# Performance work log

Measured on AMD Instinct MI355X. Metric: run time of the kernel, lower is better.

The kernel has to match this reference:

```python
import jax, jax.numpy as jnp
import numpy as np

D_TXT, D_IMG, D_C, K, N = 768, 1024, 256, 10, 200000
H, HD = 4, 64  # num_heads, head_dim (D_C = H*HD)


def _ln(x, g, b):
    m = x.mean(-1, keepdims=True)
    v = ((x - m) ** 2).mean(-1, keepdims=True)
    return (x - m) / jnp.sqrt(v + 1e-5) * g + b


def _proj(x, W, b, g, be):
    # Linear -> LayerNorm -> ReLU (the *_proj_completion blocks)
    return jax.nn.relu(_ln(x @ W.T + b, g, be))


def setup_inputs() -> dict:
    key = jax.random.key(0)
    ks = jax.random.split(key, 16)
    s = 0.02
    p = lambda i, shape: jax.random.normal(ks[i], shape, jnp.float32) * s
    z = lambda: jnp.zeros((D_C,), jnp.float32)
    o = lambda: jnp.ones((D_C,), jnp.float32)
    return {
        "query": jax.random.normal(ks[0], (D_TXT,), jnp.float32),
        "cand_text": jax.random.normal(ks[1], (N, D_TXT), jnp.float32),
        "cand_img": jax.random.normal(ks[2], (N, D_IMG), jnp.float32),
        "proto_feat": jax.random.normal(ks[3], (D_C,), jnp.float32),
        "W_txt": p(4, (D_C, D_TXT)), "b_txt": z(), "g_txt": o(), "be_txt": z(),
        "W_img": p(5, (D_C, D_IMG)), "b_img": z(), "g_img": o(), "be_img": z(),
        "Wq": p(6, (D_C, D_C)), "bq": z(),
        "Wk": p(7, (D_C, D_C)), "bk": z(),
        "Wv": p(8, (D_C, D_C)), "bv": z(),
        "Wo": p(9, (D_C, D_C)), "bo": z(),
        "g1": o(), "be1": z(),
        "W1": p(10, (4 * D_C, D_C)), "b1": jnp.zeros((4 * D_C,), jnp.float32),
        "W2": p(11, (D_C, 4 * D_C)), "b2": z(),
        "g2": o(), "be2": z(),
        "k": K,
    }


def reference(query, cand_text, cand_img, proto_feat,
              W_txt, b_txt, g_txt, be_txt,
              W_img, b_img, g_img, be_img,
              Wq, bq, Wk, bk, Wv, bv, Wo, bo,
              g1, be1, W1, b1, W2, b2, g2, be2, k):
    # ---- search_neighbors: cosine sim + topk over the available (text) DB ----
    qn = query / jnp.maximum(jnp.linalg.norm(query), 1e-12)
    cn = cand_text / jnp.maximum(
        jnp.linalg.norm(cand_text, axis=1, keepdims=True), 1e-12)
    sims = cn @ qn                                  # [N]
    _, idx = jax.lax.top_k(sims, k)                 # [k]
    neigh_txt = cand_text[idx]                      # [k, D_TXT]
    neigh_img = cand_img[idx]                       # [k, D_IMG]

    # ---- complete_feature ----
    avail_feat = _proj(query, W_txt, b_txt, g_txt, be_txt)        # [D_C]
    avail_nb = _proj(neigh_txt, W_txt, b_txt, g_txt, be_txt)      # [k, D_C]
    miss_nb = _proj(neigh_img, W_img, b_img, g_img, be_img)       # [k, D_C]

    Kmat = jnp.concatenate([proto_feat[None], avail_nb], axis=0)  # [k+1, D_C]
    Vmat = jnp.concatenate([proto_feat[None], miss_nb], axis=0)   # [k+1, D_C]

    qp = (avail_feat @ Wq.T + bq).reshape(H, HD)                  # [H, HD]
    kp = (Kmat @ Wk.T + bk).reshape(-1, H, HD)                    # [k+1, H, HD]
    vp = (Vmat @ Wv.T + bv).reshape(-1, H, HD)                    # [k+1, H, HD]
    scores = jnp.einsum('hd,nhd->hn', qp, kp) / jnp.sqrt(
        jnp.asarray(HD, jnp.float32))                             # [H, k+1]
    attn = jax.nn.softmax(scores, axis=-1)
    ctx = jnp.einsum('hn,nhd->hd', attn, vp).reshape(D_C)
    attn_out = ctx @ Wo.T + bo                                    # [D_C]

    out = _ln(attn_out + proto_feat, g1, be1)
    ffn = jax.nn.relu(out @ W1.T + b1) @ W2.T + b2
    out = _ln(ffn + out, g2, be2) + proto_feat
    return out
```

## Files before the change

kernel.cpp:

```cpp
#include <hip/hip_runtime.h>
#include <cfloat>
#include <climits>
#include <math.h>

#define N_CAND 200000
#define DTXT 768
#define DIMG 1024
#define DC 256
#define KTOP 10
#define NKV 11
#define CHUNK 2000
#define NBLK_TOPK 100

__device__ __forceinline__ float wave_sum(float v) {
#pragma unroll
  for (int off = 32; off; off >>= 1) v += __shfl_xor(v, off, 64);
  return v;
}

__global__ void k_sims(const float* __restrict__ q, const float* __restrict__ ct,
                       float* __restrict__ sims) {
  const int lane = threadIdx.x & 63;
  const int wave = threadIdx.x >> 6;
  const int row = blockIdx.x * 4 + wave;
  if (row >= N_CAND) return;
  const float4* r4 = (const float4*)(ct + (size_t)row * DTXT);
  const float4* q4 = (const float4*)q;
  float dot = 0.f, nrm = 0.f;
#pragma unroll
  for (int i = 0; i < 3; ++i) {
    float4 a = r4[lane + i * 64];
    float4 b = q4[lane + i * 64];
    dot += a.x * b.x + a.y * b.y + a.z * b.z + a.w * b.w;
    nrm += a.x * a.x + a.y * a.y + a.z * a.z + a.w * a.w;
  }
  dot = wave_sum(dot);
  nrm = wave_sum(nrm);
  if (lane == 0) sims[row] = dot / fmaxf(sqrtf(nrm), 1e-12f);
}

__device__ int block_argmax_pos(float* sv, const int* si, int M) {
  const int t = threadIdx.x;
  __shared__ float wv[4];
  __shared__ int wp[4];
  float bv = -FLT_MAX;
  int bp = -1;
  for (int j = t; j < M; j += 256) {
    float v = sv[j];
    if (bp < 0 || v > bv || (v == bv && si[j] < si[bp])) { bv = v; bp = j; }
  }
#pragma unroll
  for (int off = 32; off; off >>= 1) {
    float ov = __shfl_xor(bv, off, 64);
    int op = __shfl_xor(bp, off, 64);
    if (op >= 0 && (bp < 0 || ov > bv || (ov == bv && si[op] < si[bp]))) {
      bv = ov; bp = op;
    }
  }
  if ((t & 63) == 0) { wv[t >> 6] = bv; wp[t >> 6] = bp; }
  __syncthreads();
  if (t == 0) {
#pragma unroll
    for (int w = 1; w < 4; ++w) {
      if (wp[w] >= 0 && (wp[0] < 0 || wv[w] > wv[0] ||
                         (wv[w] == wv[0] && si[wp[w]] < si[wp[0]]))) {
        wv[0] = wv[w]; wp[0] = wp[w];
      }
    }
  }
  __syncthreads();
  int res = wp[0];
  __syncthreads();
  return res;
}

__global__ void k_topk_part(const float* __restrict__ sims,
                            float* __restrict__ cvals, int* __restrict__ cidx) {
  __shared__ float sv[CHUNK];
  __shared__ int si[CHUNK];
  const int t = threadIdx.x;
  const int lo = blockIdx.x * CHUNK;
  for (int j = t; j < CHUNK; j += 256) { sv[j] = sims[lo + j]; si[j] = lo + j; }
  __syncthreads();
  for (int r = 0; r < KTOP; ++r) {
    int p = block_argmax_pos(sv, si, CHUNK);
    if (t == 0) {
      cvals[blockIdx.x * KTOP + r] = sv[p];
      cidx[blockIdx.x * KTOP + r] = si[p];
      sv[p] = -INFINITY;
    }
    __syncthreads();
  }
}

__global__ void k_topk_final(const float* __restrict__ cvals,
                             const int* __restrict__ cidx,
                             int* __restrict__ fidx) {
  __shared__ float sv[NBLK_TOPK * KTOP];
  __shared__ int si[NBLK_TOPK * KTOP];
  const int t = threadIdx.x;
  for (int j = t; j < NBLK_TOPK * KTOP; j += 256) { sv[j] = cvals[j]; si[j] = cidx[j]; }
  __syncthreads();
  for (int r = 0; r < KTOP; ++r) {
    int p = block_argmax_pos(sv, si, NBLK_TOPK * KTOP);
    if (t == 0) { fidx[r] = si[p]; sv[p] = -INFINITY; }
    __syncthreads();
  }
}

__global__ void k_proj(const float* __restrict__ q, const float* __restrict__ ct,
                       const float* __restrict__ ci,
                       const float* __restrict__ Wt, const float* __restrict__ bt,
                       const float* __restrict__ gt, const float* __restrict__ bet,
                       const float* __restrict__ Wi, const float* __restrict__ bi,
                       const float* __restrict__ gi, const float* __restrict__ bei,
                       const int* __restrict__ fidx,
                       float* __restrict__ af, float* __restrict__ anb,
                       float* __restrict__ mnb) {
  __shared__ float x[DIMG];
  __shared__ float tmp[DC];
  __shared__ float redm, redr;
  const int t = threadIdx.x;
  const int j = blockIdx.x;
  const float *W, *b, *g, *be, *src;
  float* dst;
  int D;
  if (j == 0) {
    src = q; D = DTXT; W = Wt; b = bt; g = gt; be = bet; dst = af;
  } else if (j < 11) {
    src = ct + (size_t)fidx[j - 1] * DTXT;
    D = DTXT; W = Wt; b = bt; g = gt; be = bet; dst = anb + (j - 1) * DC;
  } else {
    src = ci + (size_t)fidx[j - 11] * DIMG;
    D = DIMG; W = Wi; b = bi; g = gi; be = bei; dst = mnb + (j - 11) * DC;
  }
  for (int d = t; d < D; d += 256) x[d] = src[d];
  __syncthreads();
  const float4* w4 = (const float4*)(W + (size_t)t * D);
  float acc = 0.f;
  for (int d4 = 0; d4 < (D >> 2); ++d4) {
    float4 w = w4[d4];
    acc += w.x * x[4 * d4] + w.y * x[4 * d4 + 1] + w.z * x[4 * d4 + 2] +
           w.w * x[4 * d4 + 3];
  }
  acc += b[t];
  tmp[t] = acc;
  __syncthreads();
  if (t < 64) {
    float s = tmp[t] + tmp[t + 64] + tmp[t + 128] + tmp[t + 192];
    s = wave_sum(s);
    if (t == 0) redm = s * (1.f / 256.f);
  }
  __syncthreads();
  if (t < 64) {
    float s = 0.f;
#pragma unroll
    for (int kk = 0; kk < 4; ++kk) {
      float d0 = tmp[t + 64 * kk] - redm;
      s += d0 * d0;
    }
    s = wave_sum(s);
    if (t == 0) redr = rsqrtf(s * (1.f / 256.f) + 1e-5f);
  }
  __syncthreads();
  float y = (acc - redm) * redr * g[t] + be[t];
  dst[t] = fmaxf(y, 0.f);
}

__global__ void __launch_bounds__(1024) k_attn_ffn(
    const float* __restrict__ proto, const float* __restrict__ Wq,
    const float* __restrict__ bq, const float* __restrict__ Wk,
    const float* __restrict__ bk, const float* __restrict__ Wv,
    const float* __restrict__ bv, const float* __restrict__ Wo,
    const float* __restrict__ bo, const float* __restrict__ g1,
    const float* __restrict__ be1, const float* __restrict__ W1,
    const float* __restrict__ b1, const float* __restrict__ W2,
    const float* __restrict__ b2, const float* __restrict__ g2,
    const float* __restrict__ be2, const float* __restrict__ af,
    const float* __restrict__ anb, const float* __restrict__ mnb,
    float* __restrict__ out) {
  __shared__ float s_af[DC];
  __shared__ float s_K[NKV * DC];
  __shared__ float s_V[NKV * DC];
  __shared__ float s_qp[DC];
  __shared__ float s_kp[NKV * DC];
  __shared__ float s_vp[NKV * DC];
  __shared__ float s_sc[4][NKV];
  __shared__ float s_at[4][NKV];
  __shared__ float s_ctx[DC];
  __shared__ float s_t[DC];
  __shared__ float s_o1[DC];
  __shared__ float s_h[4 * DC];
  __shared__ float redm, redr;
  const int t = threadIdx.x;

  if (t < DC) {
    s_af[t] = af[t];
    s_K[t] = proto[t];
    s_V[t] = proto[t];
  }
  for (int i = t; i < KTOP * DC; i += 1024) {
    s_K[DC + i] = anb[i];
    s_V[DC + i] = mnb[i];
  }
  __syncthreads();

  if (t < DC) {
    const float4* w4 = (const float4*)(Wq + (size_t)t * DC);
    float a = 0.f;
    for (int d4 = 0; d4 < DC / 4; ++d4) {
      float4 w = w4[d4];
      a += w.x * s_af[4 * d4] + w.y * s_af[4 * d4 + 1] +
           w.z * s_af[4 * d4 + 2] + w.w * s_af[4 * d4 + 3];
    }
    s_qp[t] = a + bq[t];
  }
  for (int o = t; o < NKV * DC; o += 1024) {
    int n = o >> 8, c = o & 255;
    const float4* wk4 = (const float4*)(Wk + (size_t)c * DC);
    const float4* wv4 = (const float4*)(Wv + (size_t)c * DC);
    const float* Kn = s_K + n * DC;
    const float* Vn = s_V + n * DC;
    float ak = 0.f, av = 0.f;
    for (int d4 = 0; d4 < DC / 4; ++d4) {
      float4 wk_ = wk4[d4], wv_ = wv4[d4];
      ak += wk_.x * Kn[4 * d4] + wk_.y * Kn[4 * d4 + 1] +
            wk_.z * Kn[4 * d4 + 2] + wk_.w * Kn[4 * d4 + 3];
      av += wv_.x * Vn[4 * d4] + wv_.y * Vn[4 * d4 + 1] +
            wv_.z * Vn[4 * d4 + 2] + wv_.w * Vn[4 * d4 + 3];
    }
    s_kp[o] = ak + bk[c];
    s_vp[o] = av + bv[c];
  }
  __syncthreads();

  if (t < 4 * NKV) {
    int h = t / NKV, n = t % NKV;
    const float* qh = s_qp + h * 64;
    const float* kh = s_kp + n * DC + h * 64;
    float a = 0.f;
#pragma unroll
    for (int d = 0; d < 64; ++d) a += qh[d] * kh[d];
    s_sc[h][n] = a * 0.125f;
  }
  __syncthreads();
  if (t < 4) {
    float m = -INFINITY;
    for (int n = 0; n < NKV; ++n) m = fmaxf(m, s_sc[t][n]);
    float s = 0.f;
    for (int n = 0; n < NKV; ++n) {
      float e = expf(s_sc[t][n] - m);
      s_at[t][n] = e;
      s += e;
    }
    float inv = 1.f / s;
    for (int n = 0; n < NKV; ++n) s_at[t][n] *= inv;
  }
  __syncthreads();
  if (t < DC) {
    int h = t >> 6;
    float a = 0.f;
#pragma unroll
    for (int n = 0; n < NKV; ++n) a += s_at[h][n] * s_vp[n * DC + t];
    s_ctx[t] = a;
  }
  __syncthreads();
  float myv = 0.f;
  if (t < DC) {
    const float4* w4 = (const float4*)(Wo + (size_t)t * DC);
    float a = 0.f;
    for (int d4 = 0; d4 < DC / 4; ++d4) {
      float4 w = w4[d4];
      a += w.x * s_ctx[4 * d4] + w.y * s_ctx[4 * d4 + 1] +
           w.z * s_ctx[4 * d4 + 2] + w.w * s_ctx[4 * d4 + 3];
    }
    myv = a + bo[t] + proto[t];
    s_t[t] = myv;
  }
  __syncthreads();
  if (t < 64) {
    float s = s_t[t] + s_t[t + 64] + s_t[t + 128] + s_t[t + 192];
    s = wave_sum(s);
    if (t == 0) redm = s * (1.f / 256.f);
  }
  __syncthreads();
  if (t < 64) {
    float s = 0.f;
#pragma unroll
    for (int kk = 0; kk < 4; ++kk) {
      float d0 = s_t[t + 64 * kk] - redm;
      s += d0 * d0;
    }
    s = wave_sum(s);
    if (t == 0) redr = rsqrtf(s * (1.f / 256.f) + 1e-5f);
  }
  __syncthreads();
  if (t < DC) s_o1[t] = (myv - redm) * redr * g1[t] + be1[t];
  __syncthreads();
  {
    const float4* w4 = (const float4*)(W1 + (size_t)t * DC);
    float a = 0.f;
    for (int d4 = 0; d4 < DC / 4; ++d4) {
      float4 w = w4[d4];
      a += w.x * s_o1[4 * d4] + w.y * s_o1[4 * d4 + 1] +
           w.z * s_o1[4 * d4 + 2] + w.w * s_o1[4 * d4 + 3];
    }
    s_h[t] = fmaxf(a + b1[t], 0.f);
  }
  __syncthreads();
  float myy = 0.f;
  if (t < DC) {
    const float4* w4 = (const float4*)(W2 + (size_t)t * 4 * DC);
    float a = 0.f;
    for (int d4 = 0; d4 < DC; ++d4) {
      float4 w = w4[d4];
      a += w.x * s_h[4 * d4] + w.y * s_h[4 * d4 + 1] +
           w.z * s_h[4 * d4 + 2] + w.w * s_h[4 * d4 + 3];
    }
    myy = a + b2[t] + s_o1[t];
    s_t[t] = myy;
  }
  __syncthreads();
  if (t < 64) {
    float s = s_t[t] + s_t[t + 64] + s_t[t + 128] + s_t[t + 192];
    s = wave_sum(s);
    if (t == 0) redm = s * (1.f / 256.f);
  }
  __syncthreads();
  if (t < 64) {
    float s = 0.f;
#pragma unroll
    for (int kk = 0; kk < 4; ++kk) {
      float d0 = s_t[t + 64 * kk] - redm;
      s += d0 * d0;
    }
    s = wave_sum(s);
    if (t == 0) redr = rsqrtf(s * (1.f / 256.f) + 1e-5f);
  }
  __syncthreads();
  if (t < DC) out[t] = (myy - redm) * redr * g2[t] + be2[t] + proto[t];
}

extern "C" void kernel_launch(void* const* d_in, const int* in_sizes, int n_in,
                              void* d_out, int out_size, void* d_ws,
                              size_t ws_size, hipStream_t stream) {
  (void)in_sizes; (void)n_in; (void)out_size; (void)ws_size;
  const float* query = (const float*)d_in[0];
  const float* ct    = (const float*)d_in[1];
  const float* ci    = (const float*)d_in[2];
  const float* proto = (const float*)d_in[3];
  const float* Wt    = (const float*)d_in[4];
  const float* bt    = (const float*)d_in[5];
  const float* gt    = (const float*)d_in[6];
  const float* bet   = (const float*)d_in[7];
  const float* Wi    = (const float*)d_in[8];
  const float* bi    = (const float*)d_in[9];
  const float* gi    = (const float*)d_in[10];
  const float* bei   = (const float*)d_in[11];
  const float* Wq    = (const float*)d_in[12];
  const float* bq    = (const float*)d_in[13];
  const float* Wk    = (const float*)d_in[14];
  const float* bk    = (const float*)d_in[15];
  const float* Wv    = (const float*)d_in[16];
  const float* bv    = (const float*)d_in[17];
  const float* Wo    = (const float*)d_in[18];
  const float* bo    = (const float*)d_in[19];
  const float* g1    = (const float*)d_in[20];
  const float* be1   = (const float*)d_in[21];
  const float* W1    = (const float*)d_in[22];
  const float* b1    = (const float*)d_in[23];
  const float* W2    = (const float*)d_in[24];
  const float* b2    = (const float*)d_in[25];
  const float* g2    = (const float*)d_in[26];
  const float* be2   = (const float*)d_in[27];
  float* out = (float*)d_out;

  char* ws = (char*)d_ws;
  float* sims  = (float*)(ws);
  float* cvals = (float*)(ws + 800000);
  int*   cidx  = (int*)(ws + 804000);
  int*   fidx  = (int*)(ws + 808000);
  float* af    = (float*)(ws + 808064);
  float* anb   = (float*)(ws + 809088);
  float* mnb   = (float*)(ws + 819328);

  k_sims<<<dim3(N_CAND / 4), dim3(256), 0, stream>>>(query, ct, sims);
  k_topk_part<<<dim3(NBLK_TOPK), dim3(256), 0, stream>>>(sims, cvals, cidx);
  k_topk_final<<<dim3(1), dim3(256), 0, stream>>>(cvals, cidx, fidx);
  k_proj<<<dim3(21), dim3(256), 0, stream>>>(query, ct, ci, Wt, bt, gt, bet, Wi,
                                             bi, gi, bei, fidx, af, anb, mnb);
  k_attn_ffn<<<dim3(1), dim3(1024), 0, stream>>>(
      proto, Wq, bq, Wk, bk, Wv, bv, Wo, bo, g1, be1, W1, b1, W2, b2, g2, be2,
      af, anb, mnb, out);
}
```

Before: 1.586 ms.

## Split single-block attention/FFN kernel into multi-block stage kernels

Replaces the single 1024-thread block that did QKV projection, attention, output projection and FFN with six smaller kernels. QKV runs over 23 blocks, and Wo, W1 and W2 are split across several blocks, so the matrix-vector work is spread over more compute units. The cost is extra launches and intermediate results passing through global workspace memory. The single-block tail was likely latency-bound by serial weight reads.

```diff
diff --git a/kernel.cpp b/kernel.cpp
--- a/kernel.cpp
+++ b/kernel.cpp
@@ -167,73 +167,55 @@
   dst[t] = fmaxf(y, 0.f);
 }
 
-__global__ void __launch_bounds__(1024) k_attn_ffn(
-    const float* __restrict__ proto, const float* __restrict__ Wq,
-    const float* __restrict__ bq, const float* __restrict__ Wk,
-    const float* __restrict__ bk, const float* __restrict__ Wv,
-    const float* __restrict__ bv, const float* __restrict__ Wo,
-    const float* __restrict__ bo, const float* __restrict__ g1,
-    const float* __restrict__ be1, const float* __restrict__ W1,
-    const float* __restrict__ b1, const float* __restrict__ W2,
-    const float* __restrict__ b2, const float* __restrict__ g2,
-    const float* __restrict__ be2, const float* __restrict__ af,
-    const float* __restrict__ anb, const float* __restrict__ mnb,
-    float* __restrict__ out) {
-  __shared__ float s_af[DC];
-  __shared__ float s_K[NKV * DC];
-  __shared__ float s_V[NKV * DC];
+__global__ void k_qkv(const float* __restrict__ proto,
+                      const float* __restrict__ Wq, const float* __restrict__ bq,
+                      const float* __restrict__ Wk, const float* __restrict__ bk,
+                      const float* __restrict__ Wv, const float* __restrict__ bv,
+                      const float* __restrict__ af, const float* __restrict__ anb,
+                      const float* __restrict__ mnb,
+                      float* __restrict__ qp, float* __restrict__ kp,
+                      float* __restrict__ vp) {
+  __shared__ float x[DC];
+  const int t = threadIdx.x;
+  const int j = blockIdx.x;
+  const float *W, *b, *src;
+  float* dst;
+  if (j == 0) {
+    W = Wq; b = bq; src = af; dst = qp;
+  } else if (j < 12) {
+    const int n = j - 1;
+    W = Wk; b = bk; src = (n == 0) ? proto : anb + (n - 1) * DC;
+    dst = kp + n * DC;
+  } else {
+    const int n = j - 12;
+    W = Wv; b = bv; src = (n == 0) ? proto : mnb + (n - 1) * DC;
+    dst = vp + n * DC;
+  }
+  x[t] = src[t];
+  __syncthreads();
+  const float4* w4 = (const float4*)(W + (size_t)t * DC);
+  float a = 0.f;
+  for (int d4 = 0; d4 < DC / 4; ++d4) {
+    float4 w = w4[d4];
+    a += w.x * x[4 * d4] + w.y * x[4 * d4 + 1] + w.z * x[4 * d4 + 2] +
+         w.w * x[4 * d4 + 3];
+  }
+  dst[t] = a + b[t];
+}
+
+__global__ void k_score_ctx(const float* __restrict__ qp,
+                            const float* __restrict__ kp,
+                            const float* __restrict__ vp,
+                            float* __restrict__ ctx) {
   __shared__ float s_qp[DC];
   __shared__ float s_kp[NKV * DC];
   __shared__ float s_vp[NKV * DC];
   __shared__ float s_sc[4][NKV];
   __shared__ float s_at[4][NKV];
-  __shared__ float s_ctx[DC];
-  __shared__ float s_t[DC];
-  __shared__ float s_o1[DC];
-  __shared__ float s_h[4 * DC];
-  __shared__ float redm, redr;
-  const int t = threadIdx.x;
-
-  if (t < DC) {
-    s_af[t] = af[t];
-    s_K[t] = proto[t];
-    s_V[t] = proto[t];
-  }
-  for (int i = t; i < KTOP * DC; i += 1024) {
-    s_K[DC + i] = anb[i];
-    s_V[DC + i] = mnb[i];
-  }
-  __syncthreads();
-
-  if (t < DC) {
-    const float4* w4 = (const float4*)(Wq + (size_t)t * DC);
-    float a = 0.f;
-    for (int d4 = 0; d4 < DC / 4; ++d4) {
-      float4 w = w4[d4];
-      a += w.x * s_af[4 * d4] + w.y * s_af[4 * d4 + 1] +
-           w.z * s_af[4 * d4 + 2] + w.w * s_af[4 * d4 + 3];
-    }
-    s_qp[t] = a + bq[t];
-  }
-  for (int o = t; o < NKV * DC; o += 1024) {
-    int n = o >> 8, c = o & 255;
-    const float4* wk4 = (const float4*)(Wk + (size_t)c * DC);
-    const float4* wv4 = (const float4*)(Wv + (size_t)c * DC);
-    const float* Kn = s_K + n * DC;
-    const float* Vn = s_V + n * DC;
-    float ak = 0.f, av = 0.f;
-    for (int d4 = 0; d4 < DC / 4; ++d4) {
-      float4 wk_ = wk4[d4], wv_ = wv4[d4];
-      ak += wk_.x * Kn[4 * d4] + wk_.y * Kn[4 * d4 + 1] +
-            wk_.z * Kn[4 * d4 + 2] + wk_.w * Kn[4 * d4 + 3];
-      av += wv_.x * Vn[4 * d4] + wv_.y * Vn[4 * d4 + 1] +
-            wv_.z * Vn[4 * d4 + 2] + wv_.w * Vn[4 * d4 + 3];
-    }
-    s_kp[o] = ak + bk[c];
-    s_vp[o] = av + bv[c];
-  }
-  __syncthreads();
-
+  const int t = threadIdx.x;
+  s_qp[t] = qp[t];
+  for (int i = t; i < NKV * DC; i += 256) { s_kp[i] = kp[i]; s_vp[i] = vp[i]; }
+  __syncthreads();
   if (t < 4 * NKV) {
     int h = t / NKV, n = t % NKV;
     const float* qh = s_qp + h * 64;
@@ -257,26 +239,42 @@
     for (int n = 0; n < NKV; ++n) s_at[t][n] *= inv;
   }
   __syncthreads();
-  if (t < DC) {
+  {
     int h = t >> 6;
     float a = 0.f;
 #pragma unroll
     for (int n = 0; n < NKV; ++n) a += s_at[h][n] * s_vp[n * DC + t];
-    s_ctx[t] = a;
-  }
-  __syncthreads();
-  float myv = 0.f;
-  if (t < DC) {
-    const float4* w4 = (const float4*)(Wo + (size_t)t * DC);
-    float a = 0.f;
-    for (int d4 = 0; d4 < DC / 4; ++d4) {
-      float4 w = w4[d4];
-      a += w.x * s_ctx[4 * d4] + w.y * s_ctx[4 * d4 + 1] +
-           w.z * s_ctx[4 * d4 + 2] + w.w * s_ctx[4 * d4 + 3];
-    }
-    myv = a + bo[t] + proto[t];
-    s_t[t] = myv;
-  }
+    ctx[t] = a;
+  }
+}
+
+__global__ void k_wo(const float* __restrict__ Wo, const float* __restrict__ bo,
+                     const float* __restrict__ proto,
+                     const float* __restrict__ ctx, float* __restrict__ t1) {
+  __shared__ float s_c[DC];
+  const int t = threadIdx.x;
+  ((float4*)s_c)[t] = ((const float4*)ctx)[t];
+  __syncthreads();
+  const int c = blockIdx.x * 64 + t;
+  const float4* w4 = (const float4*)(Wo + (size_t)c * DC);
+  float a = 0.f;
+  for (int d4 = 0; d4 < DC / 4; ++d4) {
+    float4 w = w4[d4];
+    a += w.x * s_c[4 * d4] + w.y * s_c[4 * d4 + 1] + w.z * s_c[4 * d4 + 2] +
+         w.w * s_c[4 * d4 + 3];
+  }
+  t1[c] = a + bo[c] + proto[c];
+}
+
+__global__ void k_ffn1(const float* __restrict__ g1, const float* __restrict__ be1,
+                       const float* __restrict__ W1, const float* __restrict__ b1,
+                       const float* __restrict__ t1, float* __restrict__ o1w,
+                       float* __restrict__ h) {
+  __shared__ float s_t[DC];
+  __shared__ float s_o1[DC];
+  __shared__ float redm, redr;
+  const int t = threadIdx.x;
+  s_t[t] = t1[t];
   __syncthreads();
   if (t < 64) {
     float s = s_t[t] + s_t[t + 64] + s_t[t + 128] + s_t[t + 192];
@@ -295,31 +293,49 @@
     if (t == 0) redr = rsqrtf(s * (1.f / 256.f) + 1e-5f);
   }
   __syncthreads();
-  if (t < DC) s_o1[t] = (myv - redm) * redr * g1[t] + be1[t];
-  __syncthreads();
-  {
-    const float4* w4 = (const float4*)(W1 + (size_t)t * DC);
+  s_o1[t] = (s_t[t] - redm) * redr * g1[t] + be1[t];
+  __syncthreads();
+  if (blockIdx.x == 0) o1w[t] = s_o1[t];
+  if (t < 128) {
+    const int o = blockIdx.x * 128 + t;
+    const float4* w4 = (const float4*)(W1 + (size_t)o * DC);
     float a = 0.f;
     for (int d4 = 0; d4 < DC / 4; ++d4) {
       float4 w = w4[d4];
       a += w.x * s_o1[4 * d4] + w.y * s_o1[4 * d4 + 1] +
            w.z * s_o1[4 * d4 + 2] + w.w * s_o1[4 * d4 + 3];
     }
-    s_h[t] = fmaxf(a + b1[t], 0.f);
-  }
-  __syncthreads();
-  float myy = 0.f;
-  if (t < DC) {
-    const float4* w4 = (const float4*)(W2 + (size_t)t * 4 * DC);
-    float a = 0.f;
-    for (int d4 = 0; d4 < DC; ++d4) {
-      float4 w = w4[d4];
-      a += w.x * s_h[4 * d4] + w.y * s_h[4 * d4 + 1] +
-           w.z * s_h[4 * d4 + 2] + w.w * s_h[4 * d4 + 3];
-    }
-    myy = a + b2[t] + s_o1[t];
-    s_t[t] = myy;
-  }
+    h[o] = fmaxf(a + b1[o], 0.f);
+  }
+}
+
+__global__ void k_ffn2(const float* __restrict__ W2, const float* __restrict__ b2,
+                       const float* __restrict__ o1w, const float* __restrict__ h,
+                       float* __restrict__ t2) {
+  __shared__ float s_h[4 * DC];
+  const int t = threadIdx.x;
+#pragma unroll
+  for (int i = 0; i < 4; ++i)
+    ((float4*)s_h)[t + 64 * i] = ((const float4*)h)[t + 64 * i];
+  __syncthreads();
+  const int c = blockIdx.x * 64 + t;
+  const float4* w4 = (const float4*)(W2 + (size_t)c * 4 * DC);
+  float a = 0.f;
+  for (int d4 = 0; d4 < DC; ++d4) {
+    float4 w = w4[d4];
+    a += w.x * s_h[4 * d4] + w.y * s_h[4 * d4 + 1] + w.z * s_h[4 * d4 + 2] +
+         w.w * s_h[4 * d4 + 3];
+  }
+  t2[c] = a + b2[c] + o1w[c];
+}
+
+__global__ void k_ln2(const float* __restrict__ g2, const float* __restrict__ be2,
+                      const float* __restrict__ proto,
+                      const float* __restrict__ t2, float* __restrict__ out) {
+  __shared__ float s_t[DC];
+  __shared__ float redm, redr;
+  const int t = threadIdx.x;
+  s_t[t] = t2[t];
   __syncthreads();
   if (t < 64) {
     float s = s_t[t] + s_t[t + 64] + s_t[t + 128] + s_t[t + 192];
@@ -338,7 +354,7 @@
     if (t == 0) redr = rsqrtf(s * (1.f / 256.f) + 1e-5f);
   }
   __syncthreads();
-  if (t < DC) out[t] = (myy - redm) * redr * g2[t] + be2[t] + proto[t];
+  out[t] = (s_t[t] - redm) * redr * g2[t] + be2[t] + proto[t];
 }
 
 extern "C" void kernel_launch(void* const* d_in, const int* in_sizes, int n_in,
@@ -383,13 +399,25 @@
   float* af    = (float*)(ws + 808064);
   float* anb   = (float*)(ws + 809088);
   float* mnb   = (float*)(ws + 819328);
+  float* qp    = (float*)(ws + 829568);
+  float* kp    = (float*)(ws + 830592);
+  float* vp    = (float*)(ws + 841856);
+  float* ctx   = (float*)(ws + 853120);
+  float* t1    = (float*)(ws + 854144);
+  float* o1w   = (float*)(ws + 855168);
+  float* h     = (float*)(ws + 856192);
+  float* t2    = (float*)(ws + 860288);
 
   k_sims<<<dim3(N_CAND / 4), dim3(256), 0, stream>>>(query, ct, sims);
   k_topk_part<<<dim3(NBLK_TOPK), dim3(256), 0, stream>>>(sims, cvals, cidx);
   k_topk_final<<<dim3(1), dim3(256), 0, stream>>>(cvals, cidx, fidx);
   k_proj<<<dim3(21), dim3(256), 0, stream>>>(query, ct, ci, Wt, bt, gt, bet, Wi,
                                              bi, gi, bei, fidx, af, anb, mnb);
-  k_attn_ffn<<<dim3(1), dim3(1024), 0, stream>>>(
-      proto, Wq, bq, Wk, bk, Wv, bv, Wo, bo, g1, be1, W1, b1, W2, b2, g2, be2,
-      af, anb, mnb, out);
-}
+  k_qkv<<<dim3(23), dim3(256), 0, stream>>>(proto, Wq, bq, Wk, bk, Wv, bv, af,
+                                            anb, mnb, qp, kp, vp);
+  k_score_ctx<<<dim3(1), dim3(256), 0, stream>>>(qp, kp, vp, ctx);
+  k_wo<<<dim3(4), dim3(64), 0, stream>>>(Wo, bo, proto, ctx, t1);
+  k_ffn1<<<dim3(8), dim3(256), 0, stream>>>(g1, be1, W1, b1, t1, o1w, h);
+  k_ffn2<<<dim3(4), dim3(64), 0, stream>>>(W2, b2, o1w, h, t2);
+  k_ln2<<<dim3(1), dim3(256), 0, stream>>>(g2, be2, proto, t2, out);
+}
```

Result: faster. 1.398 ms (-11.8%).
